# Performance work log

Measured on AMD Instinct MI355X. Metric: run time of the kernel, lower is better.

The kernel has to match this reference:

```python
import jax, jax.numpy as jnp
import numpy as np

N_GLIMPSES = 3
GS = 64          # glimpse_size
IN_C = 3         # input_channels
B, H, W = 64, 512, 512


def get_glimpses(image, loc):
    """Multi-scale glimpse extraction (tf.image.extract_glimpse, centered+normalized)
    followed by antialiased bicubic resize to GS x GS, concatenated on channels."""
    b, h, w, c = image.shape
    max_size = GS * 2 ** (N_GLIMPSES - 1)
    padded = jnp.pad(image, ((0, 0), (max_size, max_size), (max_size, max_size), (0, 0)))
    hp, wp = h + 2 * max_size, w + 2 * max_size
    # normalized+centered offsets: (-1,-1)=upper-left, (1,1)=lower-right of padded image
    center = (loc + 1.0) * 0.5 * jnp.array([hp, wp], dtype=jnp.float32)  # (y, x) per batch
    glimpses = []
    for i in range(N_GLIMPSES):
        s = GS * 2 ** i  # current crop size (python int, static)
        tl = jnp.round(center - 0.5 * s).astype(jnp.int32)
        tl = jnp.clip(tl, 0, jnp.array([hp - s, wp - s], dtype=jnp.int32))

        def slice_one(img, yx):
            return jax.lax.dynamic_slice(img, (yx[0], yx[1], 0), (s, s, c))

        g = jax.vmap(slice_one)(padded, tl)                      # [B, s, s, C]
        g = jax.image.resize(g, (b, GS, GS, c), method='cubic')  # antialiased bicubic
        glimpses.append(g)
    return jnp.concatenate(glimpses, axis=-1)  # [B, GS, GS, N_GLIMPSES*C]


def setup_inputs() -> dict:
    key = jax.random.key(0)
    ks = jax.random.split(key, 10)
    image = jax.random.uniform(ks[0], (B, H, W, IN_C), dtype=jnp.float32)
    loc = jax.random.uniform(ks[1], (B, 2), dtype=jnp.float32, minval=-1.0, maxval=1.0)
    cg = N_GLIMPSES * IN_C
    # conv1_g: full-kernel (GS x GS) valid conv -> 1x1x128
    Wg = jax.random.normal(ks[2], (GS, GS, cg, 128), dtype=jnp.float32) * (1.0 / np.sqrt(GS * GS * cg))
    bg = jnp.zeros((128,), jnp.float32)
    # conv1_l: 1x1 conv on loc [B,1,1,2]
    Wl = jax.random.normal(ks[3], (2, 128), dtype=jnp.float32) * (1.0 / np.sqrt(2.0))
    bl = jnp.zeros((128,), jnp.float32)
    # out: 1x1 conv 128 -> 256
    Wo = jax.random.normal(ks[4], (128, 256), dtype=jnp.float32) * (1.0 / np.sqrt(128.0))
    bo = jnp.zeros((256,), jnp.float32)
    return {"image": image, "loc": loc, "Wg": Wg, "bg": bg, "Wl": Wl, "bl": bl, "Wo": Wo, "bo": bo}


def reference(image, loc, Wg, bg, Wl, bl, Wo, bo):
    glimpses = get_glimpses(image, loc)  # [B, GS, GS, N_GLIMPSES*IN_C]
    # conv1_g with kernel == glimpse size and VALID padding == dense contraction over hwc
    x1 = jax.nn.relu(jnp.einsum('bhwc,hwck->bk', glimpses, Wg) + bg)  # [B,128]
    x2 = jax.nn.relu(loc @ Wl + bl)                                   # [B,128]
    out = jax.nn.relu((x1 + x2) @ Wo + bo)                            # [B,256]
    return out
```

## Files before the change

kernel.cpp:

```cpp
#include <hip/hip_runtime.h>
#include <hip/hip_bf16.h>

#define IMG_H 512
#define IMG_W 512
#define PAD   256
#define HP    1024
#define BATCH 64
#define KTOT  36864
#define KTILE 96
#define NTILES 384
#define GSTRIDE 104

typedef __attribute__((ext_vector_type(8))) short short8;
typedef __attribute__((ext_vector_type(4))) float f32x4;

__device__ __forceinline__ float keys_cubic(float x) {
  if (x >= 2.0f) return 0.0f;
  if (x >= 1.0f) return ((-0.5f * x + 2.5f) * x - 4.0f) * x + 2.0f;
  return ((1.5f * x - 2.5f) * x) * x + 1.0f;
}

__device__ __forceinline__ int iclamp(int v, int lo, int hi) {
  return min(max(v, lo), hi);
}
__device__ __forceinline__ unsigned short f2bits(float f) {
  __hip_bfloat16 h = __float2bfloat16(f);
  unsigned short s;
  __builtin_memcpy(&s, &h, 2);
  return s;
}

__global__ __launch_bounds__(256) void glimpse_kernel(
    const float* __restrict__ img, const float* __restrict__ loc,
    unsigned short* __restrict__ G) {
  __shared__ float tmp1[384];
  __shared__ float tmp2[768];
  const int y   = blockIdx.x & 63;
  const int b   = blockIdx.x >> 6;
  const int tid = threadIdx.x;

  const float cy = (loc[2 * b] + 1.0f) * 0.5f * 1024.0f;
  const float cx = (loc[2 * b + 1] + 1.0f) * 0.5f * 1024.0f;
  const int tly0 = iclamp((int)rintf(cy - 32.0f), 0, HP - 64);
  const int tlx0 = iclamp((int)rintf(cx - 32.0f), 0, HP - 64);
  const int tly1 = iclamp((int)rintf(cy - 64.0f), 0, HP - 128);
  const int tlx1 = iclamp((int)rintf(cx - 64.0f), 0, HP - 128);
  const int tly2 = iclamp((int)rintf(cy - 128.0f), 0, HP - 256);
  const int tlx2 = iclamp((int)rintf(cx - 128.0f), 0, HP - 256);
  const float* imb = img + (size_t)b * (IMG_H * IMG_W * 3);
  unsigned short* Grow = G + ((size_t)b * 64 + y) * (64 * 9);

  if (tid < 192) {
    int x = tid / 3, c = tid - 3 * (tid / 3);
    int py = tly0 + y - PAD, px = tlx0 + x - PAD;
    float v = 0.0f;
    if ((unsigned)py < (unsigned)IMG_H && (unsigned)px < (unsigned)IMG_W)
      v = imb[(py * IMG_W + px) * 3 + c];
    Grow[x * 9 + c] = f2bits(v);
  }

  float wy1[8];
  int iy0_1;
  {
    float sy = ((float)y + 0.5f) * 2.0f - 0.5f;
    iy0_1 = (int)ceilf(sy - 4.0f);
    float ws = 0.0f;
#pragma unroll
    for (int t = 0; t < 8; ++t) {
      int i = iy0_1 + t;
      float w = (i >= 0 && i < 128) ? keys_cubic(fabsf(sy - (float)i) * 0.5f) : 0.0f;
      wy1[t] = w;
      ws += w;
    }
    float wi = 1.0f / ws;
#pragma unroll
    for (int t = 0; t < 8; ++t) wy1[t] *= wi;
  }
  float wy2[16];
  int iy0_2;
  {
    float sy = ((float)y + 0.5f) * 4.0f - 0.5f;
    iy0_2 = (int)ceilf(sy - 8.0f);
    float ws = 0.0f;
#pragma unroll
    for (int t = 0; t < 16; ++t) {
      int i = iy0_2 + t;
      float w = (i >= 0 && i < 256) ? keys_cubic(fabsf(sy - (float)i) * 0.25f) : 0.0f;
      wy2[t] = w;
      ws += w;
    }
    float wi = 1.0f / ws;
#pragma unroll
    for (int t = 0; t < 16; ++t) wy2[t] *= wi;
  }

  for (int e = tid; e < 384; e += 256) {
    int x = e / 3, c = e - 3 * (e / 3);
    int px = tlx1 - PAD + x;
    float a = 0.0f;
    if ((unsigned)px < (unsigned)IMG_W) {
      const float* colp = imb + (px * 3 + c);
#pragma unroll
      for (int t = 0; t < 8; ++t) {
        int py = tly1 + iy0_1 + t - PAD;
        if ((unsigned)py < (unsigned)IMG_H)
          a = fmaf(wy1[t], colp[py * (IMG_W * 3)], a);
      }
    }
    tmp1[e] = a;
  }
  for (int e = tid; e < 768; e += 256) {
    int x = e / 3, c = e - 3 * (e / 3);
    int px = tlx2 - PAD + x;
    float a = 0.0f;
    if ((unsigned)px < (unsigned)IMG_W) {
      const float* colp = imb + (px * 3 + c);
#pragma unroll
      for (int t = 0; t < 16; ++t) {
        int py = tly2 + iy0_2 + t - PAD;
        if ((unsigned)py < (unsigned)IMG_H)
          a = fmaf(wy2[t], colp[py * (IMG_W * 3)], a);
      }
    }
    tmp2[e] = a;
  }
  __syncthreads();

  for (int o = tid; o < 384; o += 256) {
    int oo = (o >= 192) ? o - 192 : o;
    int xo = oo / 3, c = oo - 3 * xo;
    if (o < 192) {
      float sx  = ((float)xo + 0.5f) * 2.0f - 0.5f;
      int   ix0 = (int)ceilf(sx - 4.0f);
      float a = 0.0f, wsx = 0.0f;
#pragma unroll
      for (int t = 0; t < 8; ++t) {
        int i = ix0 + t;
        if (i >= 0 && i < 128) {
          float w = keys_cubic(fabsf(sx - (float)i) * 0.5f);
          wsx += w;
          a = fmaf(w, tmp1[i * 3 + c], a);
        }
      }
      Grow[xo * 9 + 3 + c] = f2bits(a / wsx);
    } else {
      float sx  = ((float)xo + 0.5f) * 4.0f - 0.5f;
      int   ix0 = (int)ceilf(sx - 8.0f);
      float a = 0.0f, wsx = 0.0f;
#pragma unroll
      for (int t = 0; t < 16; ++t) {
        int i = ix0 + t;
        if (i >= 0 && i < 256) {
          float w = keys_cubic(fabsf(sx - (float)i) * 0.25f);
          wsx += w;
          a = fmaf(w, tmp2[i * 3 + c], a);
        }
      }
      Grow[xo * 9 + 6 + c] = f2bits(a / wsx);
    }
  }
}

__global__ __launch_bounds__(256) void gemm_kernel(
    const unsigned short* __restrict__ G, const float* __restrict__ Wg,
    float* __restrict__ partials) {
  __shared__ __align__(16) unsigned short Gs[64 * GSTRIDE];
  const int tid  = threadIdx.x;
  const int tile = blockIdx.x;
  const int kt   = tile * KTILE;

  {
    const int m = tid >> 2, i = tid & 3;
    const unsigned short* src = G + (size_t)m * KTOT + kt;
    unsigned short* dst = Gs + m * GSTRIDE;
#pragma unroll
    for (int p = 0; p < 3; ++p) {
      const int o8 = (i + 4 * p) * 8;
      *(float4*)(dst + o8) = *(const float4*)(src + o8);
    }
  }
  __syncthreads();

  const int lane = tid & 63;
  const int wv   = tid >> 6;
  const int ln   = lane & 15;
  const int q    = lane >> 4;
  const int nb   = wv * 32 + ln;

  f32x4 acc[4][2];
#pragma unroll
  for (int mt = 0; mt < 4; ++mt)
#pragma unroll
    for (int nt = 0; nt < 2; ++nt) {
      acc[mt][nt][0] = 0.f; acc[mt][nt][1] = 0.f;
      acc[mt][nt][2] = 0.f; acc[mt][nt][3] = 0.f;
    }

#pragma unroll
  for (int s = 0; s < KTILE / 32; ++s) {
    short8 af[4];
#pragma unroll
    for (int mt = 0; mt < 4; ++mt)
      af[mt] = *(const short8*)(Gs + (mt * 16 + ln) * GSTRIDE + s * 32 + q * 8);
    short8 bf[2];
#pragma unroll
    for (int nt = 0; nt < 2; ++nt) {
      const float* wp = Wg + (size_t)(kt + s * 32 + q * 8) * 128 + nb + nt * 16;
      short8 v;
#pragma unroll
      for (int j = 0; j < 8; ++j) v[j] = (short)f2bits(wp[j * 128]);
      bf[nt] = v;
    }
#pragma unroll
    for (int mt = 0; mt < 4; ++mt)
#pragma unroll
      for (int nt = 0; nt < 2; ++nt)
        acc[mt][nt] = __builtin_amdgcn_mfma_f32_16x16x32_bf16(
            af[mt], bf[nt], acc[mt][nt], 0, 0, 0);
  }

#pragma unroll
  for (int mt = 0; mt < 4; ++mt)
#pragma unroll
    for (int nt = 0; nt < 2; ++nt)
#pragma unroll
      for (int i = 0; i < 4; ++i) {
        const int row = mt * 16 + q * 4 + i;
        const int col = nb + nt * 16;
        partials[((size_t)row * NTILES + tile) * 128 + col] = acc[mt][nt][i];
      }
}

__global__ __launch_bounds__(256) void finalize_kernel(
    const float* __restrict__ partials, const float* __restrict__ loc,
    const float* __restrict__ bg, const float* __restrict__ Wl,
    const float* __restrict__ bl, const float* __restrict__ Wo,
    const float* __restrict__ bo, float* __restrict__ out) {
  const int b   = blockIdx.x;
  const int tid = threadIdx.x;

  const float4* base = (const float4*)(partials + (size_t)b * NTILES * 128);
  float4 acc = make_float4(0.f, 0.f, 0.f, 0.f);
#pragma unroll 8
  for (int i = 0; i < 48; ++i) {
    float4 v = base[(size_t)i * 256 + tid];
    acc.x += v.x; acc.y += v.y; acc.z += v.z; acc.w += v.w;
  }

  __shared__ float red[8][128];
  __shared__ float h[128];
  {
    float* r = &red[tid >> 5][(tid & 31) * 4];
    r[0] = acc.x; r[1] = acc.y; r[2] = acc.z; r[3] = acc.w;
  }
  __syncthreads();
  if (tid < 128) {
    float ss = 0.0f;
#pragma unroll
    for (int g = 0; g < 8; ++g) ss += red[g][tid];
    float x1 = fmaxf(ss + bg[tid], 0.0f);
    float x2 = fmaxf(fmaf(loc[2 * b], Wl[tid],
                          fmaf(loc[2 * b + 1], Wl[128 + tid], bl[tid])),
                     0.0f);
    h[tid] = x1 + x2;
  }
  __syncthreads();
  {
    const int n = tid;
    float a = bo[n];
#pragma unroll 8
    for (int kk = 0; kk < 128; ++kk) a = fmaf(h[kk], Wo[kk * 256 + n], a);
    out[(size_t)b * 256 + n] = fmaxf(a, 0.0f);
  }
}

extern "C" void kernel_launch(void* const* d_in, const int* in_sizes, int n_in,
                              void* d_out, int out_size, void* d_ws, size_t ws_size,
                              hipStream_t stream) {
  const float* img = (const float*)d_in[0];
  const float* loc = (const float*)d_in[1];
  const float* Wg  = (const float*)d_in[2];
  const float* bg  = (const float*)d_in[3];
  const float* Wl  = (const float*)d_in[4];
  const float* bl  = (const float*)d_in[5];
  const float* Wo  = (const float*)d_in[6];
  const float* bo  = (const float*)d_in[7];
  float* out = (float*)d_out;

  char* ws = (char*)d_ws;
  unsigned short* G = (unsigned short*)ws;
  float* partials   = (float*)(ws + 2359296 * 2);

  glimpse_kernel<<<BATCH * 64, 256, 0, stream>>>(img, loc, G);
  gemm_kernel<<<NTILES, 256, 0, stream>>>(G, Wg, partials);
  finalize_kernel<<<BATCH, 256, 0, stream>>>(partials, loc, bg, Wl, bl, Wo, bo, out);
}
```

Measured before the change: 313.0 us.

## Pre-transpose weights to bf16 K-major and precompute bicubic weight tables

Adds a prep kernel that converts Wg to bf16 in an N-major/K-contiguous layout and builds the horizontal and vertical bicubic tap tables. The GEMM then loads A and B fragments directly from global memory with vector loads, dropping the LDS staging and the strided scalar fp32 conversions. The glimpse kernel reads the precomputed weights instead of evaluating the cubic kernel per element. Finalize moves to 512 threads. The extra kernel launch and its full pass over Wg are added on every call.

Result: no change. 317.5 us (+1.4%).

```diff
diff --git a/kernel.cpp b/kernel.cpp
--- a/kernel.cpp
+++ b/kernel.cpp
@@ -9,7 +9,7 @@
 #define KTOT  36864
 #define KTILE 96
 #define NTILES 384
-#define GSTRIDE 104
+#define TBLK  1152
 
 typedef __attribute__((ext_vector_type(8))) short short8;
 typedef __attribute__((ext_vector_type(4))) float f32x4;
@@ -30,14 +30,81 @@
   return s;
 }
 
+__global__ __launch_bounds__(256) void prep_kernel(
+    const float* __restrict__ Wg, unsigned short* __restrict__ Wt,
+    float* __restrict__ WT) {
+  if (blockIdx.x == TBLK) {
+    const int t = threadIdx.x;
+    if (t < 64) {
+      float sx = ((float)t + 0.5f) * 2.0f - 0.5f;
+      int ix0 = (int)ceilf(sx - 4.0f);
+      float ws = 0.0f;
+#pragma unroll
+      for (int tap = 0; tap < 8; ++tap) {
+        int i = ix0 + tap;
+        float w = (i >= 0 && i < 128) ? keys_cubic(fabsf(sx - (float)i) * 0.5f) : 0.0f;
+        WT[t * 9 + tap] = w;
+        ws += w;
+      }
+      WT[t * 9 + 8] = ws;
+    } else if (t < 128) {
+      const int xo = t - 64;
+      float sx = ((float)xo + 0.5f) * 4.0f - 0.5f;
+      int ix0 = (int)ceilf(sx - 8.0f);
+      float ws = 0.0f;
+#pragma unroll
+      for (int tap = 0; tap < 16; ++tap) {
+        int i = ix0 + tap;
+        float w = (i >= 0 && i < 256) ? keys_cubic(fabsf(sx - (float)i) * 0.25f) : 0.0f;
+        WT[576 + xo * 17 + tap] = w;
+        ws += w;
+      }
+      WT[576 + xo * 17 + 16] = ws;
+    }
+    return;
+  }
+
+  __shared__ float T[64][68];
+  const int tid = threadIdx.x;
+  const int kt  = (blockIdx.x % 576) * 64;
+  const int nt0 = (blockIdx.x / 576) * 64;
+  {
+    const int r = tid >> 4, nc = tid & 15;
+#pragma unroll
+    for (int kk = 0; kk < 4; ++kk) {
+      const int k = kk * 16 + r;
+      const float4 v = *(const float4*)(Wg + (size_t)(kt + k) * 128 + nt0 + nc * 4);
+      *(float4*)(&T[k][nc * 4]) = v;
+    }
+  }
+  __syncthreads();
+#pragma unroll
+  for (int it = 0; it < 2; ++it) {
+    const int item = tid + 256 * it;
+    const int n = item & 63, ko = item >> 6;
+    short8 o;
+#pragma unroll
+    for (int j = 0; j < 8; ++j) o[j] = (short)f2bits(T[ko * 8 + j][n]);
+    *(short8*)(Wt + (size_t)(nt0 + n) * KTOT + kt + ko * 8) = o;
+  }
+}
+
 __global__ __launch_bounds__(256) void glimpse_kernel(
     const float* __restrict__ img, const float* __restrict__ loc,
-    unsigned short* __restrict__ G) {
+    const float* __restrict__ WT, unsigned short* __restrict__ G) {
+  __shared__ __align__(16) float Ws[1664];
+  __shared__ float wv1n[8], wv2n[16];
   __shared__ float tmp1[384];
   __shared__ float tmp2[768];
   const int y   = blockIdx.x & 63;
   const int b   = blockIdx.x >> 6;
   const int tid = threadIdx.x;
+
+  {
+    const float4* src = (const float4*)WT;
+    float4* dst = (float4*)Ws;
+    for (int e = tid; e < 416; e += 256) dst[e] = src[e];
+  }
 
   const float cy = (loc[2 * b] + 1.0f) * 0.5f * 1024.0f;
   const float cx = (loc[2 * b + 1] + 1.0f) * 0.5f * 1024.0f;
@@ -58,41 +125,25 @@
       v = imb[(py * IMG_W + px) * 3 + c];
     Grow[x * 9 + c] = f2bits(v);
   }
-
-  float wy1[8];
-  int iy0_1;
-  {
-    float sy = ((float)y + 0.5f) * 2.0f - 0.5f;
-    iy0_1 = (int)ceilf(sy - 4.0f);
-    float ws = 0.0f;
-#pragma unroll
-    for (int t = 0; t < 8; ++t) {
-      int i = iy0_1 + t;
-      float w = (i >= 0 && i < 128) ? keys_cubic(fabsf(sy - (float)i) * 0.5f) : 0.0f;
-      wy1[t] = w;
-      ws += w;
-    }
-    float wi = 1.0f / ws;
-#pragma unroll
-    for (int t = 0; t < 8; ++t) wy1[t] *= wi;
-  }
-  float wy2[16];
-  int iy0_2;
-  {
-    float sy = ((float)y + 0.5f) * 4.0f - 0.5f;
-    iy0_2 = (int)ceilf(sy - 8.0f);
-    float ws = 0.0f;
-#pragma unroll
-    for (int t = 0; t < 16; ++t) {
-      int i = iy0_2 + t;
-      float w = (i >= 0 && i < 256) ? keys_cubic(fabsf(sy - (float)i) * 0.25f) : 0.0f;
-      wy2[t] = w;
-      ws += w;
-    }
-    float wi = 1.0f / ws;
-#pragma unroll
-    for (int t = 0; t < 16; ++t) wy2[t] *= wi;
-  }
+  __syncthreads();
+
+  if (tid < 8) {
+    wv1n[tid] = Ws[y * 9 + tid] * (1.0f / Ws[y * 9 + 8]);
+  } else if (tid >= 64 && tid < 80) {
+    const int t = tid - 64;
+    wv2n[t] = Ws[576 + y * 17 + t] * (1.0f / Ws[576 + y * 17 + 16]);
+  }
+  __syncthreads();
+
+  const float sy1 = ((float)y + 0.5f) * 2.0f - 0.5f;
+  const int iy0_1 = (int)ceilf(sy1 - 4.0f);
+  const float sy2 = ((float)y + 0.5f) * 4.0f - 0.5f;
+  const int iy0_2 = (int)ceilf(sy2 - 8.0f);
+  float rw1[8], rw2[16];
+#pragma unroll
+  for (int t = 0; t < 8; ++t) rw1[t] = wv1n[t];
+#pragma unroll
+  for (int t = 0; t < 16; ++t) rw2[t] = wv2n[t];
 
   for (int e = tid; e < 384; e += 256) {
     int x = e / 3, c = e - 3 * (e / 3);
@@ -104,7 +155,7 @@
       for (int t = 0; t < 8; ++t) {
         int py = tly1 + iy0_1 + t - PAD;
         if ((unsigned)py < (unsigned)IMG_H)
-          a = fmaf(wy1[t], colp[py * (IMG_W * 3)], a);
+          a = fmaf(rw1[t], colp[py * (IMG_W * 3)], a);
       }
     }
     tmp1[e] = a;
@@ -119,7 +170,7 @@
       for (int t = 0; t < 16; ++t) {
         int py = tly2 + iy0_2 + t - PAD;
         if ((unsigned)py < (unsigned)IMG_H)
-          a = fmaf(wy2[t], colp[py * (IMG_W * 3)], a);
+          a = fmaf(rw2[t], colp[py * (IMG_W * 3)], a);
       }
     }
     tmp2[e] = a;
@@ -130,57 +181,37 @@
     int oo = (o >= 192) ? o - 192 : o;
     int xo = oo / 3, c = oo - 3 * xo;
     if (o < 192) {
+      const float* wr = Ws + xo * 9;
       float sx  = ((float)xo + 0.5f) * 2.0f - 0.5f;
       int   ix0 = (int)ceilf(sx - 4.0f);
-      float a = 0.0f, wsx = 0.0f;
+      float a = 0.0f;
 #pragma unroll
       for (int t = 0; t < 8; ++t) {
-        int i = ix0 + t;
-        if (i >= 0 && i < 128) {
-          float w = keys_cubic(fabsf(sx - (float)i) * 0.5f);
-          wsx += w;
-          a = fmaf(w, tmp1[i * 3 + c], a);
-        }
-      }
-      Grow[xo * 9 + 3 + c] = f2bits(a / wsx);
+        int ic = iclamp(ix0 + t, 0, 127);
+        a = fmaf(wr[t], tmp1[ic * 3 + c], a);
+      }
+      Grow[xo * 9 + 3 + c] = f2bits(a / wr[8]);
     } else {
+      const float* wr = Ws + 576 + xo * 17;
       float sx  = ((float)xo + 0.5f) * 4.0f - 0.5f;
       int   ix0 = (int)ceilf(sx - 8.0f);
-      float a = 0.0f, wsx = 0.0f;
+      float a = 0.0f;
 #pragma unroll
       for (int t = 0; t < 16; ++t) {
-        int i = ix0 + t;
-        if (i >= 0 && i < 256) {
-          float w = keys_cubic(fabsf(sx - (float)i) * 0.25f);
-          wsx += w;
-          a = fmaf(w, tmp2[i * 3 + c], a);
-        }
-      }
-      Grow[xo * 9 + 6 + c] = f2bits(a / wsx);
+        int ic = iclamp(ix0 + t, 0, 255);
+        a = fmaf(wr[t], tmp2[ic * 3 + c], a);
+      }
+      Grow[xo * 9 + 6 + c] = f2bits(a / wr[16]);
     }
   }
 }
 
 __global__ __launch_bounds__(256) void gemm_kernel(
-    const unsigned short* __restrict__ G, const float* __restrict__ Wg,
+    const unsigned short* __restrict__ G, const unsigned short* __restrict__ Wt,
     float* __restrict__ partials) {
-  __shared__ __align__(16) unsigned short Gs[64 * GSTRIDE];
   const int tid  = threadIdx.x;
   const int tile = blockIdx.x;
   const int kt   = tile * KTILE;
-
-  {
-    const int m = tid >> 2, i = tid & 3;
-    const unsigned short* src = G + (size_t)m * KTOT + kt;
-    unsigned short* dst = Gs + m * GSTRIDE;
-#pragma unroll
-    for (int p = 0; p < 3; ++p) {
-      const int o8 = (i + 4 * p) * 8;
-      *(float4*)(dst + o8) = *(const float4*)(src + o8);
-    }
-  }
-  __syncthreads();
-
   const int lane = tid & 63;
   const int wv   = tid >> 6;
   const int ln   = lane & 15;
@@ -196,21 +227,19 @@
       acc[mt][nt][2] = 0.f; acc[mt][nt][3] = 0.f;
     }
 
+  const unsigned short* Ab = G + kt + q * 8;
+  const unsigned short* Bb = Wt + kt + q * 8;
+
 #pragma unroll
   for (int s = 0; s < KTILE / 32; ++s) {
     short8 af[4];
 #pragma unroll
     for (int mt = 0; mt < 4; ++mt)
-      af[mt] = *(const short8*)(Gs + (mt * 16 + ln) * GSTRIDE + s * 32 + q * 8);
+      af[mt] = *(const short8*)(Ab + (size_t)(mt * 16 + ln) * KTOT + s * 32);
     short8 bf[2];
 #pragma unroll
-    for (int nt = 0; nt < 2; ++nt) {
-      const float* wp = Wg + (size_t)(kt + s * 32 + q * 8) * 128 + nb + nt * 16;
-      short8 v;
-#pragma unroll
-      for (int j = 0; j < 8; ++j) v[j] = (short)f2bits(wp[j * 128]);
-      bf[nt] = v;
-    }
+    for (int nt = 0; nt < 2; ++nt)
+      bf[nt] = *(const short8*)(Bb + (size_t)(nb + nt * 16) * KTOT + s * 32);
 #pragma unroll
     for (int mt = 0; mt < 4; ++mt)
 #pragma unroll
@@ -231,7 +260,7 @@
       }
 }
 
-__global__ __launch_bounds__(256) void finalize_kernel(
+__global__ __launch_bounds__(512) void finalize_kernel(
     const float* __restrict__ partials, const float* __restrict__ loc,
     const float* __restrict__ bg, const float* __restrict__ Wl,
     const float* __restrict__ bl, const float* __restrict__ Wo,
@@ -242,12 +271,12 @@
   const float4* base = (const float4*)(partials + (size_t)b * NTILES * 128);
   float4 acc = make_float4(0.f, 0.f, 0.f, 0.f);
 #pragma unroll 8
-  for (int i = 0; i < 48; ++i) {
-    float4 v = base[(size_t)i * 256 + tid];
+  for (int i = 0; i < 24; ++i) {
+    float4 v = base[(size_t)i * 512 + tid];
     acc.x += v.x; acc.y += v.y; acc.z += v.z; acc.w += v.w;
   }
 
-  __shared__ float red[8][128];
+  __shared__ float red[16][128];
   __shared__ float h[128];
   {
     float* r = &red[tid >> 5][(tid & 31) * 4];
@@ -257,7 +286,7 @@
   if (tid < 128) {
     float ss = 0.0f;
 #pragma unroll
-    for (int g = 0; g < 8; ++g) ss += red[g][tid];
+    for (int g = 0; g < 16; ++g) ss += red[g][tid];
     float x1 = fmaxf(ss + bg[tid], 0.0f);
     float x2 = fmaxf(fmaf(loc[2 * b], Wl[tid],
                           fmaf(loc[2 * b + 1], Wl[128 + tid], bl[tid])),
@@ -265,7 +294,7 @@
     h[tid] = x1 + x2;
   }
   __syncthreads();
-  {
+  if (tid < 256) {
     const int n = tid;
     float a = bo[n];
 #pragma unroll 8
@@ -289,9 +318,12 @@
 
   char* ws = (char*)d_ws;
   unsigned short* G = (unsigned short*)ws;
-  float* partials   = (float*)(ws + 2359296 * 2);
-
-  glimpse_kernel<<<BATCH * 64, 256, 0, stream>>>(img, loc, G);
-  gemm_kernel<<<NTILES, 256, 0, stream>>>(G, Wg, partials);
-  finalize_kernel<<<BATCH, 256, 0, stream>>>(partials, loc, bg, Wl, bl, Wo, bo, out);
-}
+  float* partials   = (float*)(ws + 4718592);
+  unsigned short* Wt = (unsigned short*)(ws + 4718592 + 12582912);
+  float* WTbl       = (float*)(ws + 4718592 + 12582912 + 9437184);
+
+  prep_kernel<<<TBLK + 1, 256, 0, stream>>>(Wg, Wt, WTbl);
+  glimpse_kernel<<<BATCH * 64, 256, 0, stream>>>(img, loc, WTbl, G);
+  gemm_kernel<<<NTILES, 256, 0, stream>>>(G, Wt, partials);
+  finalize_kernel<<<BATCH, 512, 0, stream>>>(partials, loc, bg, Wl, bl, Wo, bo, out);
+}
```
